# Optimization experiments

Hardware: AMD Instinct MI355X
Metric: run time of the kernel (lower is better)

## Reference

```python
import jax, jax.numpy as jnp
import numpy as np

BS, IN_CH, SEQ = 2, 512, 1024
DK, DV, H = 64, 64, 16


def setup_inputs() -> dict:
    key = jax.random.key(0)
    ks = jax.random.split(key, 8)
    # init scales mirror the torch init lambdas
    sq = IN_CH ** (-0.5) * DK ** (-0.25)            # initQ / initK
    sv = (1.0 / 0.012) * H ** (-0.5) * IN_CH ** (-0.5) * 40 ** (-0.5)  # initV
    sl = 0.5 * H ** (-0.5)                           # initL
    inp = jax.random.normal(ks[0], (BS, IN_CH, SEQ), jnp.float32)
    mask = jnp.zeros((BS, SEQ), jnp.float32)
    Wq = jax.random.normal(ks[1], (IN_CH, DK, H), jnp.float32) * sq
    Wk = jax.random.normal(ks[2], (IN_CH, DK, H), jnp.float32) * sq
    Wv = jax.random.normal(ks[3], (IN_CH, DV, H), jnp.float32) * sv
    Wl = jax.random.normal(ks[4], (H, H), jnp.float32) * sl
    Ww = jax.random.normal(ks[5], (H, H), jnp.float32) * 0.01
    Wo = jax.random.normal(ks[6], (DV * H, IN_CH), jnp.float32) * 0.03
    alpha = jnp.full((1,), 2.0, jnp.float32)
    return {"inp": inp, "mask": mask, "Wq": Wq, "Wk": Wk, "Wv": Wv,
            "alphaq": alpha, "alphak": alpha, "alphav": alpha,
            "Wl": Wl, "Ww": Ww, "Wo": Wo}


def reference(inp, mask, Wq, Wk, Wv, alphaq, alphak, alphav, Wl, Ww, Wo):
    # inp: (b, c_in, s); projections -> (b, d, s, h)
    Q = jax.nn.sigmoid(alphaq) * jnp.einsum('bcs,cdh->bdsh', inp, Wq)
    K = jax.nn.sigmoid(alphak) * jnp.einsum('bcs,cdh->bdsh', inp, Wk)
    V = jax.nn.sigmoid(alphav) * jnp.einsum('bcs,cdh->bdsh', inp, Wv)
    # per-head attention logits: (b, sq, sk, h)
    J = jnp.einsum('bdqh,bdkh->bqkh', Q, K)
    # pre-softmax head mixing, additive mask over key positions
    EL = jnp.einsum('bqkh,hg->bqkg', J, Wl) - mask[:, None, :, None]
    W = jax.nn.softmax(EL, axis=2)  # softmax over keys (dim 2)
    # post-softmax head mixing
    U = jnp.einsum('bqkg,gv->bqkv', W, Ww)
    # attend to values: (b, sq, dv, hv) -> (b, sq, dv*hv)
    O = jnp.einsum('bqkv,bdkv->bqdv', U, V)
    O = O.reshape(O.shape[0], O.shape[1], DV * H)
    # output projection, back to (b, out_dim, s)
    resid = jnp.einsum('bqc,cd->bdq', O, Wo)
    # shortcut is identity since out_dim == in_ch
    return inp + resid
```

## Files before the change

kernel.cpp:

```cpp
#include <hip/hip_runtime.h>
#include <hip/hip_bf16.h>


#define B_S  2
#define C_INN 512
#define SEQL 1024
#define D_K  64
#define N_H  16
#define BQJ  (2 * 1024 * 1024)
#define KSL  16
#define KSO  8

typedef __attribute__((ext_vector_type(4))) float floatx4;
typedef __attribute__((ext_vector_type(8))) short short8;
typedef __attribute__((ext_vector_type(2))) unsigned int uint2v;
typedef __fp16 h2raw __attribute__((ext_vector_type(2)));
typedef _Float16 f16x4 __attribute__((ext_vector_type(4)));

static __device__ __forceinline__ float bf2f(unsigned short u) {
  union { unsigned int i; float f; } x; x.i = ((unsigned int)u) << 16; return x.f;
}
static __device__ __forceinline__ unsigned short f2bf(float f) {
  union { float f; unsigned int i; } x; x.f = f;
  return (unsigned short)((x.i + 0x7fffu + ((x.i >> 16) & 1u)) >> 16);
}
static __device__ __forceinline__ unsigned int pkh2(float a, float b) {
  h2raw r = __builtin_amdgcn_cvt_pkrtz(a, b);
  union { h2raw h; unsigned int u; } x; x.h = r; return x.u;
}
static __device__ __forceinline__ unsigned int pkbf(float a, float b) {
  return (unsigned int)f2bf(a) | ((unsigned int)f2bf(b) << 16);
}
static __device__ __forceinline__ f16x4 mkh4(unsigned int a, unsigned int b) {
  union { unsigned int u[2]; f16x4 h; } x; x.u[0] = a; x.u[1] = b; return x.h;
}

__global__ __launch_bounds__(256) void ath_tr(
    const float* __restrict__ inp, const float* __restrict__ Wq,
    const float* __restrict__ Wk,  const float* __restrict__ Wv,
    const float* __restrict__ Wo,
    unsigned short* __restrict__ inpT, unsigned short* __restrict__ WT,
    unsigned short* __restrict__ WoT)
{
  const int z = blockIdx.z;
  const float* src; unsigned short* dst; int R, C;
  if      (z == 0) { src = inp;              dst = inpT;                R = 512;  C = 1024; }
  else if (z == 1) { src = inp + 512 * 1024; dst = inpT + 1024 * 512;   R = 512;  C = 1024; }
  else if (z == 2) { src = Wq;               dst = WT;                  R = 512;  C = 1024; }
  else if (z == 3) { src = Wk;               dst = WT + 1024 * 512;     R = 512;  C = 1024; }
  else if (z == 4) { src = Wv;               dst = WT + 2 * 1024 * 512; R = 512;  C = 1024; }
  else             { src = Wo;               dst = WoT;                 R = 1024; C = 512;  }
  const int ct = blockIdx.x, rt = blockIdx.y;
  if (ct * 32 >= C || rt * 32 >= R) return;

  __shared__ float Ts[32][33];
  const int t = threadIdx.x;
  {
    const int r = t >> 3, c4 = (t & 7) * 4;
    const floatx4 g = *(const floatx4*)(src + (size_t)(rt * 32 + r) * C + ct * 32 + c4);
    Ts[r][c4 + 0] = g[0]; Ts[r][c4 + 1] = g[1];
    Ts[r][c4 + 2] = g[2]; Ts[r][c4 + 3] = g[3];
  }
  __syncthreads();
  {
    const int i = t >> 3, k4 = (t & 7) * 4;
    const unsigned int o0 = pkbf(Ts[k4 + 0][i], Ts[k4 + 1][i]);
    const unsigned int o1 = pkbf(Ts[k4 + 2][i], Ts[k4 + 3][i]);
    *(uint2v*)(dst + (size_t)(ct * 32 + i) * R + rt * 32 + k4) = (uint2v){o0, o1};
  }
}

__global__ __launch_bounds__(256) void ath_qkv(
    const unsigned short* __restrict__ inpT,
    const unsigned short* __restrict__ WT,
    const float* __restrict__ Aq,
    const float* __restrict__ Ak,
    const float* __restrict__ Av,
    unsigned short* __restrict__ ws)
{
  const int sblk = blockIdx.x;
  const int nblk = blockIdx.y;
  const int z = blockIdx.z;
  const int b = z / 3, p = z % 3;
  const float* Ap = (p == 0) ? Aq : ((p == 1) ? Ak : Av);
  const float sig = 1.0f / (1.0f + __expf(-Ap[0]));

  __shared__ __align__(16) unsigned short As[64][40];
  __shared__ __align__(16) unsigned short Bs[64][40];

  const int tid = threadIdx.x;
  const int w = tid >> 6, lane = tid & 63;
  const int l15 = lane & 15, quad = lane >> 4;
  const int srow = tid >> 2, sc8 = (tid & 3) * 8;

  floatx4 acc[4];
#pragma unroll
  for (int i = 0; i < 4; ++i) acc[i] = (floatx4){0.f, 0.f, 0.f, 0.f};

  for (int cc = 0; cc < 16; ++cc) {
    const int c0 = cc * 32;
    __syncthreads();
    *(short8*)&As[srow][sc8] =
        *(const short8*)(inpT + ((size_t)(b * 1024 + sblk * 64 + srow)) * 512 + c0 + sc8);
    *(short8*)&Bs[srow][sc8] =
        *(const short8*)(WT + ((size_t)(p * 1024 + nblk * 64 + srow)) * 512 + c0 + sc8);
    __syncthreads();
    const short8 a = *(const short8*)&As[w * 16 + l15][quad * 8];
#pragma unroll
    for (int nt = 0; nt < 4; ++nt) {
      const short8 bb = *(const short8*)&Bs[nt * 16 + l15][quad * 8];
      acc[nt] = __builtin_amdgcn_mfma_f32_16x16x32_bf16(a, bb, acc[nt], 0, 0, 0);
    }
  }

  unsigned short* out = ws + (size_t)p * ((size_t)B_S * N_H * SEQL * D_K);
#pragma unroll
  for (int nt = 0; nt < 4; ++nt) {
    const int h = l15;
    const int d = nblk * 4 + nt;
#pragma unroll
    for (int r = 0; r < 4; ++r) {
      const int s = sblk * 64 + w * 16 + quad * 4 + r;
      const float vout = acc[nt][r] * sig;
      if (p == 2) out[((size_t)((b * N_H + h) * D_K + d)) * SEQL + s] = f2bf(vout);
      else        out[((size_t)((b * N_H + h) * SEQL + s)) * D_K + d] = f2bf(vout);
    }
  }
}

__global__ __launch_bounds__(256, 3) void ath_lpartP(
    const float* __restrict__ maskp,
    const float* __restrict__ Wl,
    const unsigned short* __restrict__ qkv,
    float* __restrict__ lp,
    unsigned short* __restrict__ Pws)
{
  const int qblk = blockIdx.x;
  const int ks   = blockIdx.y;
  const int b    = blockIdx.z;
  const int tid = threadIdx.x;
  const int w = tid >> 6, lane = tid & 63;
  const int l15 = lane & 15, quad = lane >> 4;

  const unsigned short* Qf = qkv;
  const unsigned short* Kf = qkv + (size_t)B_S * N_H * SEQL * D_K;

  __shared__ unsigned int JtU[9216];

  const f16x4 wlA = mkh4(pkh2(Wl[(quad * 4 + 0) * 16 + l15], Wl[(quad * 4 + 1) * 16 + l15]),
                         pkh2(Wl[(quad * 4 + 2) * 16 + l15], Wl[(quad * 4 + 3) * 16 + l15]));
  const f16x4 idB = mkh4(pkh2((quad * 4 + 0 == l15) ? 1.f : 0.f, (quad * 4 + 1 == l15) ? 1.f : 0.f),
                         pkh2((quad * 4 + 2 == l15) ? 1.f : 0.f, (quad * 4 + 3 == l15) ? 1.f : 0.f));
  const unsigned int ONE2 = 0x3C003C00u;
  const f16x4 onesB = mkh4(ONE2, ONE2);
  const f16x4 zeroB = mkh4(0u, 0u);

  const float mreg = maskp[b * SEQL + ks * 64 + w * 16 + l15];
  const int k0 = ks * 64;
  const int kabs = k0 + w * 16 + l15;

  short8 qf0[4], qf1[4];
#pragma unroll
  for (int hh = 0; hh < 4; ++hh) {
    const unsigned short* qb =
        Qf + ((size_t)((b * N_H + w * 4 + hh) * SEQL) + qblk * 16 + l15) * D_K;
    qf0[hh] = *(const short8*)(qb + quad * 8);
    qf1[hh] = *(const short8*)(qb + 32 + quad * 8);
  }

#pragma unroll
  for (int kt = 0; kt < 4; ++kt) {
    floatx4 jc[4];
#pragma unroll
    for (int hh = 0; hh < 4; ++hh) {
      const unsigned short* kb =
          Kf + ((size_t)((b * N_H + w * 4 + hh) * SEQL) + k0 + kt * 16 + l15) * D_K;
      const short8 kf0 = *(const short8*)(kb + quad * 8);
      const short8 kf1 = *(const short8*)(kb + 32 + quad * 8);
      floatx4 c = (floatx4){0.f, 0.f, 0.f, 0.f};
      c = __builtin_amdgcn_mfma_f32_16x16x32_bf16(qf0[hh], kf0, c, 0, 0, 0);
      c = __builtin_amdgcn_mfma_f32_16x16x32_bf16(qf1[hh], kf1, c, 0, 0, 0);
      jc[hh] = c;
    }
#pragma unroll
    for (int r = 0; r < 4; ++r) {
      const int base = ((quad * 4 + r) * 64 + kt * 16 + l15) * 9 + w * 2;
      JtU[base + 0] = pkh2(jc[0][r], jc[1][r]);
      JtU[base + 1] = pkh2(jc[2][r], jc[3][r]);
    }
  }

  __syncthreads();

  unsigned int* Pu = (unsigned int*)Pws;
  floatx4 dl0 = (floatx4){0.f, 0.f, 0.f, 0.f};
  floatx4 dl1 = (floatx4){0.f, 0.f, 0.f, 0.f};
#pragma unroll 4
  for (int q = 0; q < 16; ++q) {
    const int jb = (q * 64 + w * 16 + l15) * 9 + quad * 2;
    const f16x4 bj = mkh4(JtU[jb], JtU[jb + 1]);
    floatx4 d1 = __builtin_amdgcn_mfma_f32_16x16x16f16(
        wlA, bj, (floatx4){0.f, 0.f, 0.f, 0.f}, 0, 0, 0);
    float p[4];
#pragma unroll
    for (int r = 0; r < 4; ++r) {
      const float e = fminf(fmaxf(d1[r] - mreg, -60.f), 60.f);
      p[r] = __expf(e);
    }
    const unsigned int u0 = pkh2(p[0], p[1]);
    const unsigned int u1 = pkh2(p[2], p[3]);
    const size_t pidx =
        ((size_t)(b * 1024 + qblk * 16 + q) * 1024 + kabs) * 8 + quad * 2;
    *(uint2v*)&Pu[pidx] = (uint2v){u0, u1};

    const f16x4 ap = mkh4(u0, u1);
    floatx4 dt = __builtin_amdgcn_mfma_f32_16x16x16f16(
        ap, idB, (floatx4){0.f, 0.f, 0.f, 0.f}, 0, 0, 0);
    const f16x4 a2 = mkh4(pkh2(dt[0], dt[1]), pkh2(dt[2], dt[3]));
    const f16x4 eq = (l15 == q) ? onesB : zeroB;
    if (q & 1) dl1 = __builtin_amdgcn_mfma_f32_16x16x16f16(a2, eq, dl1, 0, 0, 0);
    else       dl0 = __builtin_amdgcn_mfma_f32_16x16x16f16(a2, eq, dl0, 0, 0, 0);
  }
  const floatx4 dl = dl0 + dl1;

  *(floatx4*)(lp + ((size_t)((ks * 4 + w) * 2 + b)) * 16384 +
              (size_t)(qblk * 16 + l15) * 16 + quad * 4) = dl;
}

__global__ __launch_bounds__(256, 3) void ath_lpart(
    const float* __restrict__ maskp,
    const float* __restrict__ Wl,
    const unsigned short* __restrict__ qkv,
    float* __restrict__ lp)
{
  const int qblk = blockIdx.x;
  const int ks   = blockIdx.y;
  const int b    = blockIdx.z;
  const int tid = threadIdx.x;
  const int w = tid >> 6, lane = tid & 63;
  const int l15 = lane & 15, quad = lane >> 4;

  const unsigned short* Qf = qkv;
  const unsigned short* Kf = qkv + (size_t)B_S * N_H * SEQL * D_K;

  __shared__ unsigned int JtU[9216];

  const f16x4 wlA = mkh4(pkh2(Wl[(quad * 4 + 0) * 16 + l15], Wl[(quad * 4 + 1) * 16 + l15]),
                         pkh2(Wl[(quad * 4 + 2) * 16 + l15], Wl[(quad * 4 + 3) * 16 + l15]));
  const f16x4 idB = mkh4(pkh2((quad * 4 + 0 == l15) ? 1.f : 0.f, (quad * 4 + 1 == l15) ? 1.f : 0.f),
                         pkh2((quad * 4 + 2 == l15) ? 1.f : 0.f, (quad * 4 + 3 == l15) ? 1.f : 0.f));
  const unsigned int ONE2 = 0x3C003C00u;
  const f16x4 onesB = mkh4(ONE2, ONE2);
  const f16x4 zeroB = mkh4(0u, 0u);

  const float mreg = maskp[b * SEQL + ks * 64 + w * 16 + l15];
  const int k0 = ks * 64;

  short8 qf0[4], qf1[4];
#pragma unroll
  for (int hh = 0; hh < 4; ++hh) {
    const unsigned short* qb =
        Qf + ((size_t)((b * N_H + w * 4 + hh) * SEQL) + qblk * 16 + l15) * D_K;
    qf0[hh] = *(const short8*)(qb + quad * 8);
    qf1[hh] = *(const short8*)(qb + 32 + quad * 8);
  }

#pragma unroll
  for (int kt = 0; kt < 4; ++kt) {
    floatx4 jc[4];
#pragma unroll
    for (int hh = 0; hh < 4; ++hh) {
      const unsigned short* kb =
          Kf + ((size_t)((b * N_H + w * 4 + hh) * SEQL) + k0 + kt * 16 + l15) * D_K;
      const short8 kf0 = *(const short8*)(kb + quad * 8);
      const short8 kf1 = *(const short8*)(kb + 32 + quad * 8);
      floatx4 c = (floatx4){0.f, 0.f, 0.f, 0.f};
      c = __builtin_amdgcn_mfma_f32_16x16x32_bf16(qf0[hh], kf0, c, 0, 0, 0);
      c = __builtin_amdgcn_mfma_f32_16x16x32_bf16(qf1[hh], kf1, c, 0, 0, 0);
      jc[hh] = c;
    }
#pragma unroll
    for (int r = 0; r < 4; ++r) {
      const int base = ((quad * 4 + r) * 64 + kt * 16 + l15) * 9 + w * 2;
      JtU[base + 0] = pkh2(jc[0][r], jc[1][r]);
      JtU[base + 1] = pkh2(jc[2][r], jc[3][r]);
    }
  }

  __syncthreads();

  floatx4 dl0 = (floatx4){0.f, 0.f, 0.f, 0.f};
  floatx4 dl1 = (floatx4){0.f, 0.f, 0.f, 0.f};
#pragma unroll 4
  for (int q = 0; q < 16; ++q) {
    const int jb = (q * 64 + w * 16 + l15) * 9 + quad * 2;
    const f16x4 bj = mkh4(JtU[jb], JtU[jb + 1]);
    floatx4 d1 = __builtin_amdgcn_mfma_f32_16x16x16f16(
        wlA, bj, (floatx4){0.f, 0.f, 0.f, 0.f}, 0, 0, 0);
    float p[4];
#pragma unroll
    for (int r = 0; r < 4; ++r) {
      const float e = fminf(fmaxf(d1[r] - mreg, -60.f), 60.f);
      p[r] = __expf(e);
    }
    const f16x4 ap = mkh4(pkh2(p[0], p[1]), pkh2(p[2], p[3]));
    floatx4 dt = __builtin_amdgcn_mfma_f32_16x16x16f16(
        ap, idB, (floatx4){0.f, 0.f, 0.f, 0.f}, 0, 0, 0);
    const f16x4 a2 = mkh4(pkh2(dt[0], dt[1]), pkh2(dt[2], dt[3]));
    const f16x4 eq = (l15 == q) ? onesB : zeroB;
    if (q & 1) dl1 = __builtin_amdgcn_mfma_f32_16x16x16f16(a2, eq, dl1, 0, 0, 0);
    else       dl0 = __builtin_amdgcn_mfma_f32_16x16x16f16(a2, eq, dl0, 0, 0, 0);
  }
  const floatx4 dl = dl0 + dl1;

  *(floatx4*)(lp + ((size_t)((ks * 4 + w) * 2 + b)) * 16384 +
              (size_t)(qblk * 16 + l15) * 16 + quad * 4) = dl;
}

__global__ __launch_bounds__(256) void ath_linv(
    const float* __restrict__ lp, float* __restrict__ invl)
{
  const int t = blockIdx.x * 256 + threadIdx.x;
  const int b = t >> 14, rem = t & 16383;
  float s = 0.f;
#pragma unroll
  for (int sl = 0; sl < KSL * 4; ++sl) s += lp[(size_t)(sl * 2 + b) * 16384 + rem];
  invl[t] = 1.0f / fmaxf(s, 1e-37f);
}

__global__ __launch_bounds__(256, 3) void ath_opartP(
    const unsigned short* __restrict__ Pws,
    const float* __restrict__ Ww,
    const unsigned short* __restrict__ qkv,
    const float* __restrict__ invl,
    unsigned short* __restrict__ Obp)
{
  const int qblk = blockIdx.x;
  const int ks   = blockIdx.y;
  const int b    = blockIdx.z;
  const int tid = threadIdx.x;
  const int w = tid >> 6, lane = tid & 63;
  const int l15 = lane & 15, quad = lane >> 4;

  const unsigned short* Vf = qkv + 2 * (size_t)B_S * N_H * SEQL * D_K;

  __shared__ __align__(16) unsigned short Us[16 * 16 * 64];
  __shared__ float invls[16][16];

  invls[tid >> 4][tid & 15] =
      invl[(size_t)b * 16384 + (qblk * 16 + (tid >> 4)) * 16 + (tid & 15)];

  const f16x4 wwB = mkh4(pkh2(Ww[(quad * 4 + 0) * 16 + l15], Ww[(quad * 4 + 1) * 16 + l15]),
                         pkh2(Ww[(quad * 4 + 2) * 16 + l15], Ww[(quad * 4 + 3) * 16 + l15]));

  floatx4 oacc[4][4];
#pragma unroll
  for (int a = 0; a < 4; ++a)
#pragma unroll
    for (int d = 0; d < 4; ++d) oacc[a][d] = (floatx4){0.f, 0.f, 0.f, 0.f};

  const unsigned int* Pu = (const unsigned int*)Pws;

  __syncthreads();

  for (int rd = 0; rd < 2; ++rd) {
    const int kabs = ks * 128 + rd * 64 + w * 16 + l15;

#pragma unroll
    for (int qh = 0; qh < 2; ++qh) {
      uint2v pv[8];
#pragma unroll
      for (int qq = 0; qq < 8; ++qq) {
        const size_t pidx =
            ((size_t)(b * 1024 + qblk * 16 + qh * 8 + qq) * 1024 + kabs) * 8 + quad * 2;
        pv[qq] = *(const uint2v*)&Pu[pidx];
      }
#pragma unroll
      for (int qq = 0; qq < 8; ++qq) {
        const int q = qh * 8 + qq;
        const floatx4 iq = *(const floatx4*)&invls[q][quad * 4];
        union { unsigned int u; _Float16 h[2]; } z0, z1;
        z0.u = pv[qq][0]; z1.u = pv[qq][1];
        const f16x4 ap = mkh4(pkh2((float)z0.h[0] * iq[0], (float)z0.h[1] * iq[1]),
                              pkh2((float)z1.h[0] * iq[2], (float)z1.h[1] * iq[3]));
        floatx4 d2 = __builtin_amdgcn_mfma_f32_16x16x16f16(
            ap, wwB, (floatx4){0.f, 0.f, 0.f, 0.f}, 0, 0, 0);
        const int row = l15 * 16 + q;
        const int ch = (w * 2 + (quad >> 1)) ^ ((l15 ^ q) & 7);
        *(uint2v*)&Us[row * 64 + ch * 8 + (quad & 1) * 4] =
            (uint2v){pkbf(d2[0], d2[1]), pkbf(d2[2], d2[3])};
      }
    }

    __syncthreads();

#pragma unroll
    for (int tp = 0; tp < 2; ++tp) {
      const int kt_abs = ks * 128 + rd * 64 + tp * 32;
#pragma unroll
      for (int vv = 0; vv < 4; ++vv) {
        const int v = w * 4 + vv;
        const int ch = (tp * 4 + quad) ^ ((v ^ l15) & 7);
        const short8 ufr = *(const short8*)&Us[(v * 16 + l15) * 64 + ch * 8];
#pragma unroll
        for (int dt = 0; dt < 4; ++dt) {
          const short8 vfr = *(const short8*)(Vf +
              ((size_t)((b * N_H + v) * D_K + dt * 16 + l15)) * SEQL + kt_abs + quad * 8);
          oacc[vv][dt] = __builtin_amdgcn_mfma_f32_16x16x32_bf16(ufr, vfr, oacc[vv][dt], 0, 0, 0);
        }
      }
    }

    __syncthreads();
  }

#pragma unroll
  for (int vv = 0; vv < 4; ++vv) {
    const int v = w * 4 + vv;
#pragma unroll
    for (int dt = 0; dt < 4; ++dt) {
      const int d = dt * 16 + l15;
#pragma unroll
      for (int r = 0; r < 4; ++r) {
        const int q = qblk * 16 + quad * 4 + r;
        Obp[(size_t)ks * BQJ + ((size_t)(b * SEQL + q)) * 1024 + d * 16 + v] = f2bf(oacc[vv][dt][r]);
      }
    }
  }
}

__global__ __launch_bounds__(256, 2) void ath_opart(
    const float* __restrict__ maskp,
    const float* __restrict__ Wl,
    const float* __restrict__ Ww,
    const unsigned short* __restrict__ qkv,
    const float* __restrict__ invl,
    unsigned short* __restrict__ Obp)
{
  const int qblk = blockIdx.x;
  const int ks   = blockIdx.y;
  const int b    = blockIdx.z;
  const int tid = threadIdx.x;
  const int w = tid >> 6, lane = tid & 63;
  const int l15 = lane & 15, quad = lane >> 4;

  const unsigned short* Qf = qkv;
  const unsigned short* Kf = qkv + (size_t)B_S * N_H * SEQL * D_K;
  const unsigned short* Vf = qkv + 2 * (size_t)B_S * N_H * SEQL * D_K;

  __shared__ unsigned int JtU[9216];
  __shared__ float invls[16][16];

  invls[tid >> 4][tid & 15] =
      invl[(size_t)b * 16384 + (qblk * 16 + (tid >> 4)) * 16 + (tid & 15)];

  const f16x4 wlA = mkh4(pkh2(Wl[(quad * 4 + 0) * 16 + l15], Wl[(quad * 4 + 1) * 16 + l15]),
                         pkh2(Wl[(quad * 4 + 2) * 16 + l15], Wl[(quad * 4 + 3) * 16 + l15]));
  const f16x4 wwB = mkh4(pkh2(Ww[(quad * 4 + 0) * 16 + l15], Ww[(quad * 4 + 1) * 16 + l15]),
                         pkh2(Ww[(quad * 4 + 2) * 16 + l15], Ww[(quad * 4 + 3) * 16 + l15]));

  short8 qf0[4], qf1[4];
#pragma unroll
  for (int hh = 0; hh < 4; ++hh) {
    const unsigned short* qb =
        Qf + ((size_t)((b * N_H + w * 4 + hh) * SEQL) + qblk * 16 + l15) * D_K;
    qf0[hh] = *(const short8*)(qb + quad * 8);
    qf1[hh] = *(const short8*)(qb + 32 + quad * 8);
  }

  floatx4 oacc[4][4];
#pragma unroll
  for (int a = 0; a < 4; ++a)
#pragma unroll
    for (int d = 0; d < 4; ++d) oacc[a][d] = (floatx4){0.f, 0.f, 0.f, 0.f};

  __syncthreads();

  for (int rd = 0; rd < 2; ++rd) {
    const int k0 = ks * 128 + rd * 64;
    const float mreg = maskp[b * SEQL + k0 + w * 16 + l15];

#pragma unroll
    for (int kt = 0; kt < 4; ++kt) {
      floatx4 jc[4];
#pragma unroll
      for (int hh = 0; hh < 4; ++hh) {
        const unsigned short* kb =
            Kf + ((size_t)((b * N_H + w * 4 + hh) * SEQL) + k0 + kt * 16 + l15) * D_K;
        const short8 kf0 = *(const short8*)(kb + quad * 8);
        const short8 kf1 = *(const short8*)(kb + 32 + quad * 8);
        floatx4 c = (floatx4){0.f, 0.f, 0.f, 0.f};
        c = __builtin_amdgcn_mfma_f32_16x16x32_bf16(qf0[hh], kf0, c, 0, 0, 0);
        c = __builtin_amdgcn_mfma_f32_16x16x32_bf16(qf1[hh], kf1, c, 0, 0, 0);
        jc[hh] = c;
      }
#pragma unroll
      for (int r = 0; r < 4; ++r) {
        const int base = ((quad * 4 + r) * 64 + kt * 16 + l15) * 9 + w * 2;
        JtU[base + 0] = pkh2(jc[0][r], jc[1][r]);
        JtU[base + 1] = pkh2(jc[2][r], jc[3][r]);
      }
    }

    __syncthreads();

#pragma unroll 4
    for (int q = 0; q < 16; ++q) {
      const int jb = (q * 64 + w * 16 + l15) * 9 + quad * 2;
      const f16x4 bj = mkh4(JtU[jb], JtU[jb + 1]);
      floatx4 d1 = __builtin_amdgcn_mfma_f32_16x16x16f16(
          wlA, bj, (floatx4){0.f, 0.f, 0.f, 0.f}, 0, 0, 0);
      const floatx4 iq = *(const floatx4*)&invls[q][quad * 4];
      float p[4];
#pragma unroll
      for (int r = 0; r < 4; ++r) {
        const float e = fminf(fmaxf(d1[r] - mreg, -60.f), 60.f);
        p[r] = __expf(e) * iq[r];
      }
      const f16x4 ap = mkh4(pkh2(p[0], p[1]), pkh2(p[2], p[3]));
      floatx4 d2 = __builtin_amdgcn_mfma_f32_16x16x16f16(
          ap, wwB, (floatx4){0.f, 0.f, 0.f, 0.f}, 0, 0, 0);
      const int ub = (q * 64 + w * 16) * 9 + ((l15 + q) & 15) * 8 + quad * 2;
      *(uint2v*)&JtU[ub] = (uint2v){pkbf(d2[0], d2[1]), pkbf(d2[2], d2[3])};
    }

    __syncthreads();

    const unsigned short* JtS = (const unsigned short*)JtU;
#pragma unroll
    for (int tp = 0; tp < 2; ++tp) {
      const int kt_abs = ks * 128 + rd * 64 + tp * 32;
#pragma unroll
      for (int vv = 0; vv < 4; ++vv) {
        const int v = w * 4 + vv;
        const int wp = tp * 2 + (quad >> 1);
        const int so = (l15 * 64 + wp * 16) * 18 + ((v + l15) & 15) * 16 + (quad & 1) * 8;
        const short8 ufr = *(const short8*)&JtS[so];
#pragma unroll
        for (int dt = 0; dt < 4; ++dt) {
          const short8 vfr = *(const short8*)(Vf +
              ((size_t)((b * N_H + v) * D_K + dt * 16 + l15)) * SEQL + kt_abs + quad * 8);
          oacc[vv][dt] = __builtin_amdgcn_mfma_f32_16x16x32_bf16(ufr, vfr, oacc[vv][dt], 0, 0, 0);
        }
      }
    }

    __syncthreads();
  }

#pragma unroll
  for (int vv = 0; vv < 4; ++vv) {
    const int v = w * 4 + vv;
#pragma unroll
    for (int dt = 0; dt < 4; ++dt) {
      const int d = dt * 16 + l15;
#pragma unroll
      for (int r = 0; r < 4; ++r) {
        const int q = qblk * 16 + quad * 4 + r;
        Obp[(size_t)ks * BQJ + ((size_t)(b * SEQL + q)) * 1024 + d * 16 + v] = f2bf(oacc[vv][dt][r]);
      }
    }
  }
}

__global__ __launch_bounds__(256) void ath_osum(
    const unsigned short* __restrict__ Obp,
    unsigned short* __restrict__ Obsum)
{
  const size_t i = ((size_t)blockIdx.x * 256 + threadIdx.x) * 8;
  float a[8];
#pragma unroll
  for (int e = 0; e < 8; ++e) a[e] = 0.f;
#pragma unroll
  for (int ks = 0; ks < KSO; ++ks) {
    const short8 v = *(const short8*)(Obp + (size_t)ks * BQJ + i);
#pragma unroll
    for (int e = 0; e < 8; ++e) a[e] += bf2f((unsigned short)v[e]);
  }
  short8 o;
#pragma unroll
  for (int e = 0; e < 8; ++e) o[e] = (short)f2bf(a[e]);
  *(short8*)(Obsum + i) = o;
}

__global__ __launch_bounds__(256) void ath_out(
    const float* __restrict__ inp,
    const unsigned short* __restrict__ WoT,
    const unsigned short* __restrict__ Ob,
    float* __restrict__ out)
{
  const int qblk = blockIdx.x;
  const int cblk = blockIdx.y;
  const int b    = blockIdx.z;
  const int tid = threadIdx.x;
  const int w = tid >> 6, lane = tid & 63;
  const int l15 = lane & 15, quad = lane >> 4;

  __shared__ __align__(16) unsigned short Os[64][40];
  __shared__ __align__(16) unsigned short Wt[64][40];

  floatx4 acc[4];
#pragma unroll
  for (int i = 0; i < 4; ++i) acc[i] = (floatx4){0.f, 0.f, 0.f, 0.f};

  const int srow = tid >> 2, sj8 = (tid & 3) * 8;

  for (int jc = 0; jc < 32; ++jc) {
    const int j0 = jc * 32;
    __syncthreads();
    *(short8*)&Os[srow][sj8] =
        *(const short8*)(Ob + ((size_t)(b * SEQL + qblk * 64 + srow)) * 1024 + j0 + sj8);
    *(short8*)&Wt[srow][sj8] =
        *(const short8*)(WoT + ((size_t)(cblk * 64 + srow)) * 1024 + j0 + sj8);
    __syncthreads();
    const short8 a = *(const short8*)&Os[w * 16 + l15][quad * 8];
#pragma unroll
    for (int nt = 0; nt < 4; ++nt) {
      const short8 bb = *(const short8*)&Wt[nt * 16 + l15][quad * 8];
      acc[nt] = __builtin_amdgcn_mfma_f32_16x16x32_bf16(a, bb, acc[nt], 0, 0, 0);
    }
  }

#pragma unroll
  for (int nt = 0; nt < 4; ++nt) {
    const int co = cblk * 64 + nt * 16 + l15;
    const int qb = qblk * 64 + w * 16 + quad * 4;
    const float* ip = inp + ((size_t)(b * 512 + co)) * SEQL + qb;
    float* op = out + ((size_t)(b * 512 + co)) * SEQL + qb;
#pragma unroll
    for (int r = 0; r < 4; ++r) op[r] = acc[nt][r] + ip[r];
  }
}

extern "C" void kernel_launch(void* const* d_in, const int* in_sizes, int n_in,
                              void* d_out, int out_size, void* d_ws, size_t ws_size,
                              hipStream_t stream) {
  (void)in_sizes; (void)n_in; (void)out_size;
  const float* inp   = (const float*)d_in[0];
  const float* maskp = (const float*)d_in[1];
  const float* Wq    = (const float*)d_in[2];
  const float* Wk    = (const float*)d_in[3];
  const float* Wv    = (const float*)d_in[4];
  const float* Aq    = (const float*)d_in[5];
  const float* Ak    = (const float*)d_in[6];
  const float* Av    = (const float*)d_in[7];
  const float* Wl    = (const float*)d_in[8];
  const float* Ww    = (const float*)d_in[9];
  const float* Wo    = (const float*)d_in[10];

  const size_t MB = 1u << 20;
  unsigned short* qkv   = (unsigned short*)d_ws;
  unsigned short* Obsum = (unsigned short*)((char*)d_ws + 12 * MB);
  float*          invl  = (float*)((char*)d_ws + 16 * MB);
  unsigned short* WoT   = (unsigned short*)((char*)d_ws + 17 * MB);
  float*          lp    = (float*)((char*)d_ws + 18 * MB);
  unsigned short* WT    = (unsigned short*)((char*)d_ws + 26 * MB);
  unsigned short* inpT  = (unsigned short*)((char*)d_ws + 29 * MB);
  unsigned short* Obp   = (unsigned short*)((char*)d_ws + 18 * MB);
  unsigned short* Pws   = (unsigned short*)((char*)d_ws + 50 * MB);
  float* out = (float*)d_out;

  const bool useP = ws_size >= (size_t)114 * MB;

  ath_tr<<<dim3(32, 32, 6), 256, 0, stream>>>(inp, Wq, Wk, Wv, Wo, inpT, WT, WoT);
  ath_qkv<<<dim3(16, 16, 6), 256, 0, stream>>>(inpT, WT, Aq, Ak, Av, qkv);
  if (useP) {
    ath_lpartP<<<dim3(64, KSL, 2), 256, 0, stream>>>(maskp, Wl, qkv, lp, Pws);
    ath_linv<<<dim3(128), 256, 0, stream>>>(lp, invl);
    ath_opartP<<<dim3(64, KSO, 2), 256, 0, stream>>>(Pws, Ww, qkv, invl, Obp);
  } else {
    ath_lpart<<<dim3(64, KSL, 2), 256, 0, stream>>>(maskp, Wl, qkv, lp);
    ath_linv<<<dim3(128), 256, 0, stream>>>(lp, invl);
    ath_opart<<<dim3(64, KSO, 2), 256, 0, stream>>>(maskp, Wl, Ww, qkv, invl, Obp);
  }
  ath_osum<<<dim3(1024), 256, 0, stream>>>(Obp, Obsum);
  ath_out<<<dim3(16, 8, 2), 256, 0, stream>>>(inp, WoT, Obsum, out);
}
```

Before: 256.8 us.

## Fuse split-K partial-sum reduction into output projection; split opartP over d halves

Removes the separate ath_osum kernel and has ath_out read and sum the eight split-K bf16 partial buffers directly while staging its A tile. ath_opartP now splits the value dimension into two halves across blockIdx.z, which doubles the grid and halves the accumulator registers per block. This drops one launch and the Obsum write/read round trip. In exchange, ath_out re-reads the partials once for each of its 8 output-channel blocks, and opartP re-reads P and rebuilds U twice as often.

After: 258.5 us. About the same (+0.7%).

```diff
diff --git a/kernel.cpp b/kernel.cpp
--- a/kernel.cpp
+++ b/kernel.cpp
@@ -337,7 +337,8 @@
 {
   const int qblk = blockIdx.x;
   const int ks   = blockIdx.y;
-  const int b    = blockIdx.z;
+  const int z    = blockIdx.z;
+  const int b = z >> 1, dh = z & 1;
   const int tid = threadIdx.x;
   const int w = tid >> 6, lane = tid & 63;
   const int l15 = lane & 15, quad = lane >> 4;
@@ -353,11 +354,11 @@
   const f16x4 wwB = mkh4(pkh2(Ww[(quad * 4 + 0) * 16 + l15], Ww[(quad * 4 + 1) * 16 + l15]),
                          pkh2(Ww[(quad * 4 + 2) * 16 + l15], Ww[(quad * 4 + 3) * 16 + l15]));
 
-  floatx4 oacc[4][4];
+  floatx4 oacc[4][2];
 #pragma unroll
   for (int a = 0; a < 4; ++a)
 #pragma unroll
-    for (int d = 0; d < 4; ++d) oacc[a][d] = (floatx4){0.f, 0.f, 0.f, 0.f};
+    for (int d = 0; d < 2; ++d) oacc[a][d] = (floatx4){0.f, 0.f, 0.f, 0.f};
 
   const unsigned int* Pu = (const unsigned int*)Pws;
 
@@ -403,9 +404,10 @@
         const int ch = (tp * 4 + quad) ^ ((v ^ l15) & 7);
         const short8 ufr = *(const short8*)&Us[(v * 16 + l15) * 64 + ch * 8];
 #pragma unroll
-        for (int dt = 0; dt < 4; ++dt) {
+        for (int dt = 0; dt < 2; ++dt) {
+          const int dtile = dh * 2 + dt;
           const short8 vfr = *(const short8*)(Vf +
-              ((size_t)((b * N_H + v) * D_K + dt * 16 + l15)) * SEQL + kt_abs + quad * 8);
+              ((size_t)((b * N_H + v) * D_K + dtile * 16 + l15)) * SEQL + kt_abs + quad * 8);
           oacc[vv][dt] = __builtin_amdgcn_mfma_f32_16x16x32_bf16(ufr, vfr, oacc[vv][dt], 0, 0, 0);
         }
       }
@@ -418,8 +420,8 @@
   for (int vv = 0; vv < 4; ++vv) {
     const int v = w * 4 + vv;
 #pragma unroll
-    for (int dt = 0; dt < 4; ++dt) {
-      const int d = dt * 16 + l15;
+    for (int dt = 0; dt < 2; ++dt) {
+      const int d = (dh * 2 + dt) * 16 + l15;
 #pragma unroll
       for (int r = 0; r < 4; ++r) {
         const int q = qblk * 16 + quad * 4 + r;
@@ -563,30 +565,10 @@
   }
 }
 
-__global__ __launch_bounds__(256) void ath_osum(
-    const unsigned short* __restrict__ Obp,
-    unsigned short* __restrict__ Obsum)
-{
-  const size_t i = ((size_t)blockIdx.x * 256 + threadIdx.x) * 8;
-  float a[8];
-#pragma unroll
-  for (int e = 0; e < 8; ++e) a[e] = 0.f;
-#pragma unroll
-  for (int ks = 0; ks < KSO; ++ks) {
-    const short8 v = *(const short8*)(Obp + (size_t)ks * BQJ + i);
-#pragma unroll
-    for (int e = 0; e < 8; ++e) a[e] += bf2f((unsigned short)v[e]);
-  }
-  short8 o;
-#pragma unroll
-  for (int e = 0; e < 8; ++e) o[e] = (short)f2bf(a[e]);
-  *(short8*)(Obsum + i) = o;
-}
-
 __global__ __launch_bounds__(256) void ath_out(
     const float* __restrict__ inp,
     const unsigned short* __restrict__ WoT,
-    const unsigned short* __restrict__ Ob,
+    const unsigned short* __restrict__ Obp,
     float* __restrict__ out)
 {
   const int qblk = blockIdx.x;
@@ -608,8 +590,24 @@
   for (int jc = 0; jc < 32; ++jc) {
     const int j0 = jc * 32;
     __syncthreads();
-    *(short8*)&Os[srow][sj8] =
-        *(const short8*)(Ob + ((size_t)(b * SEQL + qblk * 64 + srow)) * 1024 + j0 + sj8);
+    {
+      const size_t obase = ((size_t)(b * SEQL + qblk * 64 + srow)) * 1024 + j0 + sj8;
+      short8 pv[KSO];
+#pragma unroll
+      for (int ksb = 0; ksb < KSO; ++ksb)
+        pv[ksb] = *(const short8*)(Obp + (size_t)ksb * BQJ + obase);
+      float a[8];
+#pragma unroll
+      for (int e = 0; e < 8; ++e) a[e] = 0.f;
+#pragma unroll
+      for (int ksb = 0; ksb < KSO; ++ksb)
+#pragma unroll
+        for (int e = 0; e < 8; ++e) a[e] += bf2f((unsigned short)pv[ksb][e]);
+      short8 o;
+#pragma unroll
+      for (int e = 0; e < 8; ++e) o[e] = (short)f2bf(a[e]);
+      *(short8*)&Os[srow][sj8] = o;
+    }
     *(short8*)&Wt[srow][sj8] =
         *(const short8*)(WoT + ((size_t)(cblk * 64 + srow)) * 1024 + j0 + sj8);
     __syncthreads();
@@ -650,7 +648,6 @@
 
   const size_t MB = 1u << 20;
   unsigned short* qkv   = (unsigned short*)d_ws;
-  unsigned short* Obsum = (unsigned short*)((char*)d_ws + 12 * MB);
   float*          invl  = (float*)((char*)d_ws + 16 * MB);
   unsigned short* WoT   = (unsigned short*)((char*)d_ws + 17 * MB);
   float*          lp    = (float*)((char*)d_ws + 18 * MB);
@@ -667,12 +664,11 @@
   if (useP) {
     ath_lpartP<<<dim3(64, KSL, 2), 256, 0, stream>>>(maskp, Wl, qkv, lp, Pws);
     ath_linv<<<dim3(128), 256, 0, stream>>>(lp, invl);
-    ath_opartP<<<dim3(64, KSO, 2), 256, 0, stream>>>(Pws, Ww, qkv, invl, Obp);
+    ath_opartP<<<dim3(64, KSO, 4), 256, 0, stream>>>(Pws, Ww, qkv, invl, Obp);
   } else {
     ath_lpart<<<dim3(64, KSL, 2), 256, 0, stream>>>(maskp, Wl, qkv, lp);
     ath_linv<<<dim3(128), 256, 0, stream>>>(lp, invl);
     ath_opart<<<dim3(64, KSO, 2), 256, 0, stream>>>(maskp, Wl, Ww, qkv, invl, Obp);
   }
-  ath_osum<<<dim3(1024), 256, 0, stream>>>(Obp, Obsum);
-  ath_out<<<dim3(16, 8, 2), 256, 0, stream>>>(inp, WoT, Obsum, out);
-}
+  ath_out<<<dim3(16, 8, 2), 256, 0, stream>>>(inp, WoT, Obp, out);
+}
```
